# Kernel optimization log

Measured on AMD Instinct MI355X. Metric: run time of the kernel, lower is better.

The kernel has to match this reference:

```python
import jax, jax.numpy as jnp
import numpy as np
import math

# ---- static configuration (mirrors init_kwargs) ----
NQ = 8            # n_qubits (main register)
NA = 2            # n_ancilla = ceil(log2(n_select))
NSEL = 4          # n_select
DEG = 3           # degree
LAYERS = 2        # n_ansatz_layers
KLOC = 2          # k_local
LATENT = 128
B = 256
NROTS = 4 * NQ * LAYERS          # 64
GROUPS = [(s, s + 1) for s in range(NQ - KLOC + 1)]  # sliding 2-local -> 7 groups
NOBS = len(GROUPS)
KDIM = 2 ** KLOC                  # 4
C64 = jnp.complex64
TWO_PI = 2.0 * math.pi

CNOT = jnp.array([[1, 0, 0, 0], [0, 1, 0, 0], [0, 0, 0, 1], [0, 0, 1, 0]], dtype=C64)

# ---- gate matrices (theta may be traced) ----
def ry_mat(th):
    c = jnp.cos(th / 2).astype(C64); s = jnp.sin(th / 2).astype(C64)
    return jnp.stack([jnp.stack([c, -s]), jnp.stack([s, c])])

def rz_mat(th):
    return jnp.diag(jnp.stack([jnp.exp(-0.5j * th), jnp.exp(0.5j * th)])).astype(C64)

def crx_mat(th):
    c = jnp.cos(th / 2).astype(C64); isn = (-1j * jnp.sin(th / 2)).astype(C64)
    one = jnp.ones((), C64)
    m = jnp.zeros((4, 4), C64)
    m = m.at[0, 0].set(one).at[1, 1].set(one)
    m = m.at[2, 2].set(c).at[3, 3].set(c).at[2, 3].set(isn).at[3, 2].set(isn)
    return m

# ---- state-vector gate application (state: (2,)*rank, wire = axis) ----
def apply_1q(state, U, w):
    return jnp.moveaxis(jnp.tensordot(U, state, axes=((1,), (w,))), 0, w)

def apply_2q(state, U, w0, w1):
    st = jnp.tensordot(U.reshape(2, 2, 2, 2), state, axes=((2, 3), (w0, w1)))
    return jnp.moveaxis(st, (0, 1), (w0, w1))

def _sim14_ops(nq, layers):
    ops, idx = [], 0
    for _ in range(layers):
        for i in range(nq):
            ops.append(("ry", (i,), idx)); idx += 1
        for i in range(nq - 1, -1, -1):
            ops.append(("crx", (i, (i + 1) % nq), idx)); idx += 1
        for i in range(nq):
            ops.append(("ry", (i,), idx)); idx += 1
        for i in [nq - 1] + list(range(nq - 1)):
            ops.append(("crx", (i, (i - 1) % nq), idx)); idx += 1
    return ops

def apply_sim14(state, p, layers, adjoint=False):
    ops = _sim14_ops(NQ, layers)
    seq = list(reversed(ops)) if adjoint else ops
    sgn = -1.0 if adjoint else 1.0
    for kind, ws, idx in seq:
        th = sgn * p[idx]
        if kind == "ry":
            state = apply_1q(state, ry_mat(th), ws[0])
        else:
            state = apply_2q(state, crx_mat(th), ws[0], ws[1])
    return state

def pcphase(state, phi):
    # e^{+i phi} on ancilla=|0..0> subspace (first 2^NQ states in (anc, main) ordering), e^{-i phi} elsewhere
    sr = state.reshape(2 ** NQ, 2 ** NA)
    ph = jnp.where(jnp.arange(2 ** NA) == 0, jnp.exp(1j * phi), jnp.exp(-1j * phi)).astype(C64)
    return (sr * ph[None, :]).reshape(state.shape)

def prepare(state, prep_p, adjoint=False):
    if not adjoint:
        for ly in range(NA):          # n_prep_layers == n_ancilla
            for qi in range(NA):
                state = apply_1q(state, ry_mat(prep_p[ly, qi, 0]), NQ + qi)
                state = apply_1q(state, rz_mat(prep_p[ly, qi, 1]), NQ + qi)
            for i in range(NA - 1):
                state = apply_2q(state, CNOT, NQ + i, NQ + i + 1)
    else:
        for ly in reversed(range(NA)):
            for i in reversed(range(NA - 1)):
                state = apply_2q(state, CNOT, NQ + i, NQ + i + 1)
            for qi in reversed(range(NA)):
                state = apply_1q(state, rz_mat(-prep_p[ly, qi, 1]), NQ + qi)
                state = apply_1q(state, ry_mat(-prep_p[ly, qi, 0]), NQ + qi)
    return state

def select(state, ts, adjoint=False):
    # ancilla wires (NQ, NQ+1) are the trailing axes; flattened index == control value s
    sr = state.reshape((2,) * NQ + (2 ** NA,))
    for s in range(NSEL):
        sub = apply_sim14(sr[..., s], ts[s], LAYERS, adjoint=adjoint)
        sr = sr.at[..., s].set(sub)
    return sr.reshape(state.shape)

def create_hermitian(A, Bp, D, N):
    h = jnp.zeros((N, N), C64)
    count = 0
    for i in range(1, N):
        h = h.at[i - 1, i - 1].set(D[i].astype(C64))
        for j in range(i):
            h = h.at[i, j].set((A[count + j] + 1j * Bp[count + j]).astype(C64))
        count += i
    return h + h.conj().T

def simulate(ts, prep_p, sig, qff, H_all):
    # ts: (NSEL, NROTS) for one batch element
    state = jnp.zeros((2,) * (NQ + NA), C64).at[(0,) * (NQ + NA)].set(1.0)
    state = pcphase(state, sig[0])
    for k in range(DEG):
        state = prepare(state, prep_p)
        state = select(state, ts, adjoint=(k % 2 == 1))
        state = prepare(state, prep_p, adjoint=True)
        state = pcphase(state, sig[k + 1])
    state = apply_sim14(state, qff, 1)
    es = []
    for w, (a, b) in enumerate(GROUPS):
        hpsi = apply_2q(state, H_all[w], a, b)
        es.append(jnp.real(jnp.vdot(state, hpsi)))
    return jnp.stack(es).astype(jnp.float32)  # (NOBS,)

def linear(x, w, b):
    return x @ w.T + b

def sinusoidal_embedding(t, dim):
    half = dim // 2
    freqs = jnp.exp(-math.log(10000.0) * jnp.arange(half, dtype=jnp.float32) / half)
    args = t[:, None] * freqs[None]
    return jnp.concatenate([jnp.cos(args), jnp.sin(args)], axis=-1)

def _forward(z_t, t, te_w1, te_b1, te_w2, te_b2, ip_w1, ip_b1, ip_w2, ip_b2,
             prep_params, signal_angles, qff_params, A_obs, B_obs, D_obs, head_w, head_b):
    t_emb = sinusoidal_embedding(t, LATENT)
    t_emb = linear(jax.nn.silu(linear(t_emb, te_w1, te_b1)), te_w2, te_b2)
    h = jnp.concatenate([z_t, t_emb], axis=-1)
    h = linear(jax.nn.silu(linear(h, ip_w1, ip_b1)), ip_w2, ip_b2)
    ts = jax.nn.sigmoid(h).reshape(z_t.shape[0], NSEL, NROTS) * TWO_PI
    H_all = jax.vmap(lambda a, b, d: create_hermitian(a, b, d, KDIM))(A_obs, B_obs, D_obs)  # (NOBS,4,4)
    expvals = jax.vmap(simulate, in_axes=(0, None, None, None, None))(
        ts, prep_params, signal_angles, qff_params, H_all)  # (B, NOBS)
    return linear(expvals, head_w, head_b)  # (B, LATENT)

def setup_inputs() -> dict:
    key = jax.random.key(0)
    ks = jax.random.split(key, 16)
    def n(k, shape, s=0.05):
        return s * jax.random.normal(k, shape, jnp.float32)
    return {
        "z_t": jax.random.normal(ks[0], (B, LATENT), jnp.float32),
        "t": jax.random.uniform(ks[1], (B,), jnp.float32),
        "te_w1": n(ks[2], (LATENT, LATENT)), "te_b1": jnp.zeros((LATENT,), jnp.float32),
        "te_w2": n(ks[3], (LATENT, LATENT)), "te_b2": jnp.zeros((LATENT,), jnp.float32),
        "ip_w1": n(ks[4], (2 * LATENT, 2 * LATENT)), "ip_b1": jnp.zeros((2 * LATENT,), jnp.float32),
        "ip_w2": n(ks[5], (NSEL * NROTS, 2 * LATENT)), "ip_b2": jnp.zeros((NSEL * NROTS,), jnp.float32),
        "prep_params": 0.1 * jax.random.normal(ks[6], (NA, NA, 2), jnp.float32),
        "signal_angles": 0.1 * jax.random.normal(ks[7], (DEG + 1,), jnp.float32),
        "qff_params": jax.random.uniform(ks[8], (4 * NQ,), jnp.float32),
        "A_obs": 2.0 * jax.random.normal(ks[9], (NOBS, KDIM * (KDIM - 1) // 2), jnp.float32),
        "B_obs": 2.0 * jax.random.normal(ks[10], (NOBS, KDIM * (KDIM - 1) // 2), jnp.float32),
        "D_obs": 2.0 * jax.random.normal(ks[11], (NOBS, KDIM), jnp.float32),
        "head_w": n(ks[12], (LATENT, NOBS)), "head_b": jnp.zeros((LATENT,), jnp.float32),
    }

def reference(z_t, t, te_w1, te_b1, te_w2, te_b2, ip_w1, ip_b1, ip_w2, ip_b2,
              prep_params, signal_angles, qff_params, A_obs, B_obs, D_obs, head_w, head_b):
    return _forward(z_t, t, te_w1, te_b1, te_w2, te_b2, ip_w1, ip_b1, ip_w2, ip_b2,
                    prep_params, signal_angles, qff_params, A_obs, B_obs, D_obs, head_w, head_b)
```

## Files before the change

kernel.cpp:

```cpp
#include <hip/hip_runtime.h>
#include <math.h>

#define NOBS 7
#define PI_F 3.14159265358979f


template<int LM>
__device__ __forceinline__ float lane_partner(float x) {
  if constexpr (LM == 1) {
    return __int_as_float(__builtin_amdgcn_mov_dpp(__float_as_int(x), 0xB1, 0xF, 0xF, true));
  } else if constexpr (LM == 2) {
    return __int_as_float(__builtin_amdgcn_mov_dpp(__float_as_int(x), 0x4E, 0xF, 0xF, true));
  } else if constexpr (LM == 4) {
    int a = __builtin_amdgcn_mov_dpp(__float_as_int(x), 0x1B, 0xF, 0xF, true);
    return __int_as_float(__builtin_amdgcn_mov_dpp(a, 0x141, 0xF, 0xF, true));
  } else if constexpr (LM == 8) {
    int a = __builtin_amdgcn_mov_dpp(__float_as_int(x), 0x141, 0xF, 0xF, true);
    return __int_as_float(__builtin_amdgcn_mov_dpp(a, 0x140, 0xF, 0xF, true));
  } else if constexpr (LM == 16) {
#if __has_builtin(__builtin_amdgcn_permlane16_swap)
    unsigned xu = __float_as_uint(x);
    auto r = __builtin_amdgcn_permlane16_swap(xu, xu, false, false);
    return (__uint_as_float(r[0]) + __uint_as_float(r[1])) - x;
#else
    return __shfl_xor(x, 16, 64);
#endif
  } else {
#if __has_builtin(__builtin_amdgcn_permlane32_swap)
    unsigned xu = __float_as_uint(x);
    auto r = __builtin_amdgcn_permlane32_swap(xu, xu, false, false);
    return (__uint_as_float(r[0]) + __uint_as_float(r[1])) - x;
#else
    return __shfl_xor(x, 32, 64);
#endif
  }
}

template<int LM>
__device__ __forceinline__ float xor_sum(float x) {
  if constexpr (LM == 16) {
#if __has_builtin(__builtin_amdgcn_permlane16_swap)
    unsigned xu = __float_as_uint(x);
    auto r = __builtin_amdgcn_permlane16_swap(xu, xu, false, false);
    return __uint_as_float(r[0]) + __uint_as_float(r[1]);
#else
    return x + __shfl_xor(x, 16, 64);
#endif
  } else if constexpr (LM == 32) {
#if __has_builtin(__builtin_amdgcn_permlane32_swap)
    unsigned xu = __float_as_uint(x);
    auto r = __builtin_amdgcn_permlane32_swap(xu, xu, false, false);
    return __uint_as_float(r[0]) + __uint_as_float(r[1]);
#else
    return x + __shfl_xor(x, 32, 64);
#endif
  } else {
    return x + lane_partner<LM>(x);
  }
}

__device__ __forceinline__ float rdlane(float v, int idx) {
  return __int_as_float(__builtin_amdgcn_readlane(__float_as_int(v), idx));
}

__device__ __forceinline__ float2 cmul(float2 a, float2 b) {
  return make_float2(a.x*b.x - a.y*b.y, a.x*b.y + a.y*b.x);
}
__device__ __forceinline__ float2 cmulc(float2 a, float2 b) {
  return make_float2(a.x*b.x + a.y*b.y, a.y*b.x - a.x*b.y);
}
__device__ __forceinline__ float2 cadd(float2 a, float2 b) {
  return make_float2(a.x + b.x, a.y + b.y);
}

struct S4 { float r0, r1, i0, i1; };

__device__ __forceinline__ float4 wexch(int site, int wv, int lane,
                                        const float* vr, const float* vi) {
  extern __shared__ float4 dxw[];
  float4* buf = dxw + (site & 1) * 512;
  buf[wv * 64 + lane] = make_float4(vr[0], vr[1], vi[0], vi[1]);
  __syncthreads();
  return buf[(wv ^ 4) * 64 + lane];
}


template<int W>
__device__ __forceinline__ void ry_lane_g(float* vr, float* vi, int lane,
                                          float ct, float st, int idx, float sg) {
  float c = rdlane(ct, idx), s = sg * rdlane(st, idx);
  constexpr int LM = 1 << (5 - W);
  const float ls = (lane & LM) ? s : -s;
#pragma unroll
  for (int r = 0; r < 2; ++r) {
    float pr = lane_partner<LM>(vr[r]);
    float pi = lane_partner<LM>(vi[r]);
    vr[r] = c*vr[r] + ls*pr;
    vi[r] = c*vi[r] + ls*pi;
  }
}

__device__ __forceinline__ void ry_wave6_g(float* vr, float* vi, int wv, int lane, int h,
                                           float ct, float st, int idx, float sg, int site) {
  float c = rdlane(ct, idx), s = sg * rdlane(st, idx);
  float4 P = wexch(site, wv, lane, vr, vi);
  const float ls = h ? s : -s;
  vr[0] = c*vr[0] + ls*P.x;  vr[1] = c*vr[1] + ls*P.y;
  vi[0] = c*vi[0] + ls*P.z;  vi[1] = c*vi[1] + ls*P.w;
}

__device__ __forceinline__ void ry_reg7_g(float* vr, float* vi,
                                          float ct, float st, int idx, float sg) {
  float c = rdlane(ct, idx), s = sg * rdlane(st, idx);
  float a0 = vr[0], a1 = vr[1];
  vr[0] = c*a0 - s*a1;  vr[1] = s*a0 + c*a1;
  float b0 = vi[0], b1 = vi[1];
  vi[0] = c*b0 - s*b1;  vi[1] = s*b0 + c*b1;
}

template<int C, int T>
__device__ __forceinline__ void crx_ll_g(float* vr, float* vi, int lane,
                                         float ct, float st, int idx, float sg) {
  float c = rdlane(ct, idx), s = sg * rdlane(st, idx);
  constexpr int LC = 1 << (5 - C), LT = 1 << (5 - T);
  const bool act = (lane & LC) != 0;
  const float cp = act ? c : 1.f, sp = act ? s : 0.f;
#pragma unroll
  for (int r = 0; r < 2; ++r) {
    float pr = lane_partner<LT>(vr[r]);
    float pi = lane_partner<LT>(vi[r]);
    vr[r] = cp*vr[r] + sp*pi;
    vi[r] = cp*vi[r] - sp*pr;
  }
}

template<int T>
__device__ __forceinline__ void crx_7l_g(float* vr, float* vi,
                                         float ct, float st, int idx, float sg) {
  float c = rdlane(ct, idx), s = sg * rdlane(st, idx);
  constexpr int LT = 1 << (5 - T);
  float pr = lane_partner<LT>(vr[1]);
  float pi = lane_partner<LT>(vi[1]);
  vr[1] = c*vr[1] + s*pi;
  vi[1] = c*vi[1] - s*pr;
}

template<int C>
__device__ __forceinline__ void crx_l7_g(float* vr, float* vi, int lane,
                                         float ct, float st, int idx, float sg) {
  float c = rdlane(ct, idx), s = sg * rdlane(st, idx);
  constexpr int LC = 1 << (5 - C);
  const bool act = (lane & LC) != 0;
  const float cp = act ? c : 1.f, sp = act ? s : 0.f;
  float xr = vr[0], xi = vi[0], yr = vr[1], yi = vi[1];
  vr[0] = cp*xr + sp*yi;  vi[0] = cp*xi - sp*yr;
  vr[1] = cp*yr + sp*xi;  vi[1] = cp*yi - sp*xr;
}

template<int C>
__device__ __forceinline__ void crx_l6_g(float* vr, float* vi, int wv, int lane,
                                         float ct, float st, int idx, float sg, int site) {
  float c = rdlane(ct, idx), s = sg * rdlane(st, idx);
  float4 P = wexch(site, wv, lane, vr, vi);
  constexpr int LC = 1 << (5 - C);
  const bool act = (lane & LC) != 0;
  const float cp = act ? c : 1.f, sp = act ? s : 0.f;
  vr[0] = cp*vr[0] + sp*P.z;  vi[0] = cp*vi[0] - sp*P.x;
  vr[1] = cp*vr[1] + sp*P.w;  vi[1] = cp*vi[1] - sp*P.y;
}

__device__ __forceinline__ void crx_67_g(float* vr, float* vi, int h,
                                         float ct, float st, int idx, float sg) {
  if (h) {
    float c = rdlane(ct, idx), s = sg * rdlane(st, idx);
    float xr = vr[0], xi = vi[0], yr = vr[1], yi = vi[1];
    vr[0] = c*xr + s*yi;  vi[0] = c*xi - s*yr;
    vr[1] = c*yr + s*xi;  vi[1] = c*yi - s*xr;
  }
}

template<int T>
__device__ __forceinline__ void crx_6l_g(float* vr, float* vi, int h,
                                         float ct, float st, int idx, float sg) {
  if (h) {
    float c = rdlane(ct, idx), s = sg * rdlane(st, idx);
    constexpr int LT = 1 << (5 - T);
#pragma unroll
    for (int r = 0; r < 2; ++r) {
      float pr = lane_partner<LT>(vr[r]);
      float pi = lane_partner<LT>(vi[r]);
      vr[r] = c*vr[r] + s*pi;
      vi[r] = c*vi[r] - s*pr;
    }
  }
}

__device__ __forceinline__ void trio_fwd(float* vr, float* vi, int wv, int lane, int h,
                                         float ct, float st, int ia, int ib, int ic,
                                         float sg, int site) {
  float ca = rdlane(ct, ia), sa = sg * rdlane(st, ia);
  float cb = rdlane(ct, ib), sb = sg * rdlane(st, ib);
  float cc = rdlane(ct, ic), sc = sg * rdlane(st, ic);
  float4 P = wexch(site, wv, lane, vr, vi);
  const float lsa = h ? sa : -sa;
  float bor0 = ca*vr[0] + lsa*P.x, boi0 = ca*vi[0] + lsa*P.z;
  float bor1 = ca*vr[1] + lsa*P.y, boi1 = ca*vi[1] + lsa*P.w;
  float bpr0 = ca*P.x - lsa*vr[0], bpi0 = ca*P.z - lsa*vi[0];
  float bpr1 = ca*P.y - lsa*vr[1], bpi1 = ca*P.w - lsa*vi[1];
  float cor0 = cb*bor0 - sb*bor1, coi0 = cb*boi0 - sb*boi1;
  float cor1 = sb*bor0 + cb*bor1, coi1 = sb*boi0 + cb*boi1;
  float cpr1 = sb*bpr0 + cb*bpr1, cpi1 = sb*bpi0 + cb*bpi1;
  vr[0] = cor0;                 vi[0] = coi0;
  vr[1] = cc*cor1 + sc*cpi1;    vi[1] = cc*coi1 - sc*cpr1;
}

__device__ __forceinline__ void trio_adj(float* vr, float* vi, int wv, int lane, int h,
                                         float ct, float st, int ia, int ib, int ic,
                                         float sg, int site) {
  float ca = rdlane(ct, ia), sa = sg * rdlane(st, ia);
  float cb = rdlane(ct, ib), sb = sg * rdlane(st, ib);
  float cc = rdlane(ct, ic), sc = sg * rdlane(st, ic);
  float4 P = wexch(site, wv, lane, vr, vi);
  float dor1 = cc*vr[1] + sc*P.w,   doi1 = cc*vi[1] - sc*P.y;
  float dpr1 = cc*P.y + sc*vi[1],   dpi1 = cc*P.w - sc*vr[1];
  float eor0 = cb*vr[0] - sb*dor1,  eoi0 = cb*vi[0] - sb*doi1;
  float eor1 = sb*vr[0] + cb*dor1,  eoi1 = sb*vi[0] + cb*doi1;
  float epr0 = cb*P.x  - sb*dpr1,   epi0 = cb*P.z  - sb*dpi1;
  float epr1 = sb*P.x  + cb*dpr1,   epi1 = sb*P.z  + cb*dpi1;
  const float lsa = h ? sa : -sa;
  vr[0] = ca*eor0 + lsa*epr0;  vi[0] = ca*eoi0 + lsa*epi0;
  vr[1] = ca*eor1 + lsa*epr1;  vi[1] = ca*eoi1 + lsa*epi1;
}


__device__ __noinline__ S4 sim14_fwd(S4 v, float ct, float st, int off, int site0) {
  const int tid = threadIdx.x;
  const int lane = tid & 63, wv = tid >> 6, h = wv >> 2;
  float vr[2] = {v.r0, v.r1}, vi[2] = {v.i0, v.i1};
  const float sg = 1.f;
  ry_lane_g<0>(vr,vi,lane,ct,st,off+0,sg); ry_lane_g<1>(vr,vi,lane,ct,st,off+1,sg);
  ry_lane_g<2>(vr,vi,lane,ct,st,off+2,sg); ry_lane_g<3>(vr,vi,lane,ct,st,off+3,sg);
  ry_lane_g<4>(vr,vi,lane,ct,st,off+4,sg); ry_lane_g<5>(vr,vi,lane,ct,st,off+5,sg);
  ry_wave6_g(vr,vi,wv,lane,h,ct,st,off+6,sg,site0+0);
  ry_reg7_g(vr,vi,ct,st,off+7,sg);
  crx_7l_g<0>(vr,vi,ct,st,off+8,sg);
  crx_67_g(vr,vi,h,ct,st,off+9,sg);
  crx_l6_g<5>(vr,vi,wv,lane,ct,st,off+10,sg,site0+1);
  crx_ll_g<4,5>(vr,vi,lane,ct,st,off+11,sg); crx_ll_g<3,4>(vr,vi,lane,ct,st,off+12,sg);
  crx_ll_g<2,3>(vr,vi,lane,ct,st,off+13,sg); crx_ll_g<1,2>(vr,vi,lane,ct,st,off+14,sg);
  crx_ll_g<0,1>(vr,vi,lane,ct,st,off+15,sg);
  ry_lane_g<0>(vr,vi,lane,ct,st,off+16,sg); ry_lane_g<1>(vr,vi,lane,ct,st,off+17,sg);
  ry_lane_g<2>(vr,vi,lane,ct,st,off+18,sg); ry_lane_g<3>(vr,vi,lane,ct,st,off+19,sg);
  ry_lane_g<4>(vr,vi,lane,ct,st,off+20,sg); ry_lane_g<5>(vr,vi,lane,ct,st,off+21,sg);
  trio_fwd(vr,vi,wv,lane,h,ct,st,off+22,off+23,off+24,sg,site0+2);
  crx_l7_g<0>(vr,vi,lane,ct,st,off+25,sg);
  crx_ll_g<1,0>(vr,vi,lane,ct,st,off+26,sg); crx_ll_g<2,1>(vr,vi,lane,ct,st,off+27,sg);
  crx_ll_g<3,2>(vr,vi,lane,ct,st,off+28,sg); crx_ll_g<4,3>(vr,vi,lane,ct,st,off+29,sg);
  crx_ll_g<5,4>(vr,vi,lane,ct,st,off+30,sg);
  crx_6l_g<5>(vr,vi,h,ct,st,off+31,sg);
  return {vr[0], vr[1], vi[0], vi[1]};
}

__device__ __noinline__ S4 sim14_adj(S4 v, float ct, float st, int off, int site0) {
  const int tid = threadIdx.x;
  const int lane = tid & 63, wv = tid >> 6, h = wv >> 2;
  float vr[2] = {v.r0, v.r1}, vi[2] = {v.i0, v.i1};
  const float sg = -1.f;
  crx_6l_g<5>(vr,vi,h,ct,st,off+31,sg);
  crx_ll_g<5,4>(vr,vi,lane,ct,st,off+30,sg); crx_ll_g<4,3>(vr,vi,lane,ct,st,off+29,sg);
  crx_ll_g<3,2>(vr,vi,lane,ct,st,off+28,sg); crx_ll_g<2,1>(vr,vi,lane,ct,st,off+27,sg);
  crx_ll_g<1,0>(vr,vi,lane,ct,st,off+26,sg);
  crx_l7_g<0>(vr,vi,lane,ct,st,off+25,sg);
  trio_adj(vr,vi,wv,lane,h,ct,st,off+22,off+23,off+24,sg,site0+0);
  ry_lane_g<5>(vr,vi,lane,ct,st,off+21,sg); ry_lane_g<4>(vr,vi,lane,ct,st,off+20,sg);
  ry_lane_g<3>(vr,vi,lane,ct,st,off+19,sg); ry_lane_g<2>(vr,vi,lane,ct,st,off+18,sg);
  ry_lane_g<1>(vr,vi,lane,ct,st,off+17,sg); ry_lane_g<0>(vr,vi,lane,ct,st,off+16,sg);
  crx_ll_g<0,1>(vr,vi,lane,ct,st,off+15,sg); crx_ll_g<1,2>(vr,vi,lane,ct,st,off+14,sg);
  crx_ll_g<2,3>(vr,vi,lane,ct,st,off+13,sg); crx_ll_g<3,4>(vr,vi,lane,ct,st,off+12,sg);
  crx_ll_g<4,5>(vr,vi,lane,ct,st,off+11,sg);
  crx_l6_g<5>(vr,vi,wv,lane,ct,st,off+10,sg,site0+1);
  crx_67_g(vr,vi,h,ct,st,off+9,sg);
  crx_7l_g<0>(vr,vi,ct,st,off+8,sg);
  ry_reg7_g(vr,vi,ct,st,off+7,sg);
  ry_wave6_g(vr,vi,wv,lane,h,ct,st,off+6,sg,site0+2);
  ry_lane_g<5>(vr,vi,lane,ct,st,off+5,sg); ry_lane_g<4>(vr,vi,lane,ct,st,off+4,sg);
  ry_lane_g<3>(vr,vi,lane,ct,st,off+3,sg); ry_lane_g<2>(vr,vi,lane,ct,st,off+2,sg);
  ry_lane_g<1>(vr,vi,lane,ct,st,off+1,sg); ry_lane_g<0>(vr,vi,lane,ct,st,off+0,sg);
  return {vr[0], vr[1], vi[0], vi[1]};
}


template<int IN, int NP, int MODE>
__device__ __forceinline__ void mlp_layer(const float* __restrict__ W,
    const float* __restrict__ bias, const float* xl, float* yl,
    int rbase, int lane)
{
  const int sub = lane & 7;
  const int g   = lane >> 3;
#pragma unroll
  for (int p = 0; p < NP; ++p) {
    const int row = rbase + p * 8 + g;
    const float4* w4 = (const float4*)(W + row * IN) + sub;
    const float4* x4 = (const float4*)xl + sub;
    float acc = 0.f;
#pragma unroll
    for (int it = 0; it < IN / 32; ++it) {
      float4 w = w4[it * 8], e = x4[it * 8];
      acc += w.x*e.x + w.y*e.y + w.z*e.z + w.w*e.w;
    }
    acc = xor_sum<1>(acc);
    acc = xor_sum<2>(acc);
    acc = xor_sum<4>(acc);
    if (sub == 0) {
      float a = acc + bias[row];
      if constexpr (MODE == 0) {
        yl[row] = a / (1.f + __expf(-a));
      } else if constexpr (MODE == 1) {
        yl[row] = a;
      } else {
        float th = PI_F / (1.f + __expf(-a));
        float sn, cn;
        __sincosf(th, &sn, &cn);
        ((float2*)yl)[row] = make_float2(cn, sn);
      }
    }
  }
}


__global__ __launch_bounds__(512) void qsvt_kernel(
    const float* __restrict__ z_t, const float* __restrict__ t,
    const float* __restrict__ te_w1, const float* __restrict__ te_b1,
    const float* __restrict__ te_w2, const float* __restrict__ te_b2,
    const float* __restrict__ ip_w1, const float* __restrict__ ip_b1,
    const float* __restrict__ ip_w2, const float* __restrict__ ip_b2,
    const float* __restrict__ prep_p, const float* __restrict__ sig,
    const float* __restrict__ qff,
    const float* __restrict__ A_obs, const float* __restrict__ B_obs,
    const float* __restrict__ D_obs,
    const float* __restrict__ head_w, const float* __restrict__ head_b,
    float* __restrict__ out)
{
  __shared__ __align__(16) float emb[128];
  __shared__ __align__(16) float y1[128];
  __shared__ __align__(16) float hbuf[256];
  __shared__ __align__(16) float h1[256];
  __shared__ __align__(16) float2 seltab[256];
  __shared__ __align__(16) float2 qtab2[32];
  __shared__ __align__(16) float2 sX1[16], sX2[16], sF[16], sa0[4];
  __shared__ __align__(16) float dumpR[4][256];
  __shared__ __align__(16) float dumpI[4][256];
  __shared__ float redbuf[NOBS][4];
  __shared__ float hdc[NOBS][3], hxc[NOBS][6], hyc[NOBS][6];
  __shared__ __align__(16) float shw[128 * NOBS];
  __shared__ __align__(16) float shb[128];
  extern __shared__ float4 dxw[];

  const int tid  = threadIdx.x;
  const int lane = tid & 63;
  const int wv   = tid >> 6;
  const int s    = wv & 3;
  const int h    = wv >> 2;
  const int b    = blockIdx.x;

  if (tid < 32) {
    float sn, cn;
    __sincosf(0.5f * qff[tid], &sn, &cn);
    qtab2[tid] = make_float2(cn, sn);
  }
  if (wv == 0) {
    float2 Ga[2][2][2], Gb[2][2][2];
    for (int ly = 0; ly < 2; ++ly)
      for (int qi = 0; qi < 2; ++qi) {
        float y = prep_p[ly*4 + qi*2 + 0], z = prep_p[ly*4 + qi*2 + 1];
        float cy, sy, cz, sz;
        __sincosf(0.5f*y, &sy, &cy);
        __sincosf(0.5f*z, &sz, &cz);
        float2 g00 = make_float2( cy*cz, -cy*sz);
        float2 g01 = make_float2(-sy*cz,  sy*sz);
        float2 g10 = make_float2( sy*cz,  sy*sz);
        float2 g11 = make_float2( cy*cz,  cy*sz);
        if (qi == 0) { Ga[ly][0][0]=g00; Ga[ly][0][1]=g01; Ga[ly][1][0]=g10; Ga[ly][1][1]=g11; }
        else         { Gb[ly][0][0]=g00; Gb[ly][0][1]=g01; Gb[ly][1][0]=g10; Gb[ly][1][1]=g11; }
      }
    float2 M[2][4][4];
    for (int ly = 0; ly < 2; ++ly) {
      float2 T[4][4];
      for (int i = 0; i < 4; ++i)
        for (int j = 0; j < 4; ++j)
          T[i][j] = cmul(Ga[ly][i>>1][j>>1], Gb[ly][i&1][j&1]);
      for (int j = 0; j < 4; ++j) {
        M[ly][0][j] = T[0][j]; M[ly][1][j] = T[1][j];
        M[ly][2][j] = T[3][j]; M[ly][3][j] = T[2][j];
      }
    }
    float2 U[4][4];
    for (int i = 0; i < 4; ++i)
      for (int j = 0; j < 4; ++j) {
        float2 acc = make_float2(0.f, 0.f);
        for (int kk = 0; kk < 4; ++kk) acc = cadd(acc, cmul(M[1][i][kk], M[0][kk][j]));
        U[i][j] = acc;
      }
    float c0n, s0n, c1, s1v, c2, s2v, c3, s3v;
    __sincosf(sig[0], &s0n, &c0n);
    __sincosf(sig[1], &s1v, &c1);
    __sincosf(sig[2], &s2v, &c2);
    __sincosf(sig[3], &s3v, &c3);
    if (lane < 16) {
      int i = lane >> 2, j = lane & 3;
      float2 a1 = make_float2(0.f, 0.f), a2 = make_float2(0.f, 0.f);
      for (int k = 0; k < 4; ++k) {
        float2 tt = cmulc(U[i][k], U[j][k]);
        float sk = (k == 0) ? 1.f : -1.f;
        a1 = cadd(a1, cmul(tt, make_float2(c1, sk*s1v)));
        a2 = cadd(a2, cmul(tt, make_float2(c2, sk*s2v)));
      }
      sX1[lane] = a1;
      sX2[lane] = a2;
      float2 d3 = make_float2(c3, (i == 0) ? s3v : -s3v);
      sF[lane] = cmul(d3, make_float2(U[j][i].x, -U[j][i].y));
    }
    if (lane < 4) sa0[lane] = cmul(U[lane][0], make_float2(c0n, s0n));
  }

  if (tid < 128) {
    float fr = __expf(-9.210340371976184f * (float)(tid & 63) / 64.f);
    float arg = t[b] * fr;
    float sn, cn;
    __sincosf(arg, &sn, &cn);
    emb[tid] = (tid < 64) ? cn : sn;
  }
  __syncthreads();

  mlp_layer<128, 2, 0>(te_w1, te_b1, emb, y1, wv * 16, lane);
  if (tid < 128) hbuf[tid] = z_t[b * 128 + tid];
  __syncthreads();

  mlp_layer<128, 2, 1>(te_w2, te_b2, y1, hbuf + 128, wv * 16, lane);
  __syncthreads();

  mlp_layer<256, 4, 0>(ip_w1, ip_b1, hbuf, h1, wv * 32, lane);
  __syncthreads();

  mlp_layer<256, 4, 2>(ip_w2, ip_b2, h1, (float*)seltab, wv * 32, lane);

  if (tid < NOBS * 6)      { hxc[tid/6][tid%6] = A_obs[tid]; hyc[tid/6][tid%6] = B_obs[tid]; }
  else if (tid >= 64 && tid < 64 + NOBS*3) { int q = tid - 64; hdc[q/3][q%3] = 2.f * D_obs[(q/3)*4 + (q%3) + 1]; }
#pragma unroll
  for (int i = tid; i < 128*NOBS; i += 512) shw[i] = head_w[i];
  if (tid < 128) shb[tid] = head_b[tid];
  __syncthreads();

  float2 mycs = seltab[(s << 6) | lane];
  float selc = mycs.x, sels = mycs.y;
  float2 myq = qtab2[lane & 31];
  float qc = myq.x, qs = myq.y;

  S4 v;
  v.r0 = 0.f; v.r1 = 0.f; v.i0 = 0.f; v.i1 = 0.f;
  if (lane == 0 && h == 0) {
    float2 a0 = sa0[s];
    v.r0 = a0.x; v.i0 = a0.y;
  }

  auto ancmix = [&](const float2* R, int site) {
    float4* buf = dxw + (site & 1) * 512;
    buf[wv * 64 + lane] = make_float4(v.r0, v.r1, v.i0, v.i1);
    __syncthreads();
    float2 o0 = make_float2(0.f, 0.f), o1 = make_float2(0.f, 0.f);
#pragma unroll
    for (int sp = 0; sp < 4; ++sp) {
      float4 P = buf[(h * 4 + sp) * 64 + lane];
      float2 Rr = R[sp];
      o0 = cadd(o0, cmul(Rr, make_float2(P.x, P.z)));
      o1 = cadd(o1, cmul(Rr, make_float2(P.y, P.w)));
    }
    v.r0 = o0.x; v.i0 = o0.y; v.r1 = o1.x; v.i1 = o1.y;
  };

  v = sim14_fwd(v, selc, sels, 0, 0);
  v = sim14_fwd(v, selc, sels, 32, 3);
  ancmix(&sX1[s << 2], 6);
  v = sim14_adj(v, selc, sels, 32, 7);
  v = sim14_adj(v, selc, sels, 0, 10);
  ancmix(&sX2[s << 2], 13);
  v = sim14_fwd(v, selc, sels, 0, 14);
  v = sim14_fwd(v, selc, sels, 32, 17);
  ancmix(&sF[s << 2], 20);
  v = sim14_fwd(v, qc, qs, 0, 21);

  *(float2*)&dumpR[s][(lane << 2) | (h << 1)] = make_float2(v.r0, v.r1);
  *(float2*)&dumpI[s][(lane << 2) | (h << 1)] = make_float2(v.i0, v.i1);
  __syncthreads();

  const int w0 = h ? 4 : 0, w1 = h ? NOBS : 4;
  for (int w = w0; w < w1; ++w) {
    const int pb = 6 - w;
    int g = lane;
    int ib = ((g >> pb) << (pb + 2)) | (g & ((1 << pb) - 1));
    float xr[4], xi[4];
#pragma unroll
    for (int i = 0; i < 4; ++i) { xr[i] = dumpR[s][ib + (i << pb)]; xi[i] = dumpI[s][ib + (i << pb)]; }
    float a = hdc[w][0] * (xr[0]*xr[0] + xi[0]*xi[0])
            + hdc[w][1] * (xr[1]*xr[1] + xi[1]*xi[1])
            + hdc[w][2] * (xr[2]*xr[2] + xi[2]*xi[2]);
    const int oi[6] = {1, 2, 2, 3, 3, 3};
    const int oj[6] = {0, 0, 1, 0, 1, 2};
#pragma unroll
    for (int k2 = 0; k2 < 6; ++k2) {
      int i = oi[k2], j = oj[k2];
      float rr = xr[i]*xr[j] + xi[i]*xi[j];
      float ii = xr[i]*xi[j] - xi[i]*xr[j];
      a += 2.f * (hxc[w][k2]*rr - hyc[w][k2]*ii);
    }
    a = xor_sum<32>(a);
    a = xor_sum<16>(a);
    a = xor_sum<8>(a);
    a = xor_sum<4>(a);
    a = xor_sum<2>(a);
    a = xor_sum<1>(a);
    if (lane == 0) redbuf[w][s] = a;
  }
  __syncthreads();

  if (tid < 128) {
    float acc = shb[tid];
#pragma unroll
    for (int w = 0; w < NOBS; ++w) {
      float ev = redbuf[w][0] + redbuf[w][1] + redbuf[w][2] + redbuf[w][3];
      acc += ev * shw[tid*NOBS + w];
    }
    out[b * 128 + tid] = acc;
  }
}

extern "C" void kernel_launch(void* const* d_in, const int* in_sizes, int n_in,
                              void* d_out, int out_size, void* d_ws, size_t ws_size,
                              hipStream_t stream) {
  (void)n_in; (void)out_size; (void)d_ws; (void)ws_size;
  const float* z_t    = (const float*)d_in[0];
  const float* t      = (const float*)d_in[1];
  const float* te_w1  = (const float*)d_in[2];
  const float* te_b1  = (const float*)d_in[3];
  const float* te_w2  = (const float*)d_in[4];
  const float* te_b2  = (const float*)d_in[5];
  const float* ip_w1  = (const float*)d_in[6];
  const float* ip_b1  = (const float*)d_in[7];
  const float* ip_w2  = (const float*)d_in[8];
  const float* ip_b2  = (const float*)d_in[9];
  const float* prep_p = (const float*)d_in[10];
  const float* sig    = (const float*)d_in[11];
  const float* qff    = (const float*)d_in[12];
  const float* A_obs  = (const float*)d_in[13];
  const float* B_obs  = (const float*)d_in[14];
  const float* D_obs  = (const float*)d_in[15];
  const float* head_w = (const float*)d_in[16];
  const float* head_b = (const float*)d_in[17];
  float* out = (float*)d_out;

  int B = in_sizes[1];
  size_t dyn = 2 * 512 * sizeof(float4);
  qsvt_kernel<<<B, 512, dyn, stream>>>(
      z_t, t, te_w1, te_b1, te_w2, te_b2, ip_w1, ip_b1, ip_w2, ip_b2,
      prep_p, sig, qff, A_obs, B_obs, D_obs, head_w, head_b, out);
}
```

Baseline: 125.2 us.

## Map each select branch to a single wave with four amplitudes per lane

Switches from 8 waves (two per select branch) to 4 waves per block. Each lane now holds four amplitudes, so qubits 6 and 7 live in registers. The LDS exchanges and block-wide barriers needed for gates on qubit 6 are gone, along with the barrier before the observable stage. MLP layers now give each wave twice as many rows, which trades thread-level parallelism and raises register pressure in the serial MLP phase.

After: 126.5 us. Within noise of the previous version (+1.0%).

```diff
diff --git a/kernel.cpp b/kernel.cpp
--- a/kernel.cpp
+++ b/kernel.cpp
@@ -73,26 +73,17 @@
   return make_float2(a.x + b.x, a.y + b.y);
 }
 
-struct S4 { float r0, r1, i0, i1; };
-
-__device__ __forceinline__ float4 wexch(int site, int wv, int lane,
-                                        const float* vr, const float* vi) {
-  extern __shared__ float4 dxw[];
-  float4* buf = dxw + (site & 1) * 512;
-  buf[wv * 64 + lane] = make_float4(vr[0], vr[1], vi[0], vi[1]);
-  __syncthreads();
-  return buf[(wv ^ 4) * 64 + lane];
-}
+struct S8 { float r[4]; float i[4]; };
 
 
 template<int W>
-__device__ __forceinline__ void ry_lane_g(float* vr, float* vi, int lane,
-                                          float ct, float st, int idx, float sg) {
+__device__ __forceinline__ void ry_lane4(float* vr, float* vi, int lane,
+                                         float ct, float st, int idx, float sg) {
   float c = rdlane(ct, idx), s = sg * rdlane(st, idx);
   constexpr int LM = 1 << (5 - W);
   const float ls = (lane & LM) ? s : -s;
 #pragma unroll
-  for (int r = 0; r < 2; ++r) {
+  for (int r = 0; r < 4; ++r) {
     float pr = lane_partner<LM>(vr[r]);
     float pi = lane_partner<LM>(vi[r]);
     vr[r] = c*vr[r] + ls*pr;
@@ -100,33 +91,39 @@
   }
 }
 
-__device__ __forceinline__ void ry_wave6_g(float* vr, float* vi, int wv, int lane, int h,
-                                           float ct, float st, int idx, float sg, int site) {
-  float c = rdlane(ct, idx), s = sg * rdlane(st, idx);
-  float4 P = wexch(site, wv, lane, vr, vi);
-  const float ls = h ? s : -s;
-  vr[0] = c*vr[0] + ls*P.x;  vr[1] = c*vr[1] + ls*P.y;
-  vi[0] = c*vi[0] + ls*P.z;  vi[1] = c*vi[1] + ls*P.w;
-}
-
-__device__ __forceinline__ void ry_reg7_g(float* vr, float* vi,
-                                          float ct, float st, int idx, float sg) {
-  float c = rdlane(ct, idx), s = sg * rdlane(st, idx);
-  float a0 = vr[0], a1 = vr[1];
-  vr[0] = c*a0 - s*a1;  vr[1] = s*a0 + c*a1;
-  float b0 = vi[0], b1 = vi[1];
-  vi[0] = c*b0 - s*b1;  vi[1] = s*b0 + c*b1;
+__device__ __forceinline__ void ry_reg6(float* vr, float* vi,
+                                        float ct, float st, int idx, float sg) {
+  float c = rdlane(ct, idx), s = sg * rdlane(st, idx);
+#pragma unroll
+  for (int k = 0; k < 2; ++k) {
+    float a0 = vr[k], a1 = vr[k + 2];
+    vr[k] = c*a0 - s*a1;  vr[k + 2] = s*a0 + c*a1;
+    float b0 = vi[k], b1 = vi[k + 2];
+    vi[k] = c*b0 - s*b1;  vi[k + 2] = s*b0 + c*b1;
+  }
+}
+
+__device__ __forceinline__ void ry_reg7(float* vr, float* vi,
+                                        float ct, float st, int idx, float sg) {
+  float c = rdlane(ct, idx), s = sg * rdlane(st, idx);
+#pragma unroll
+  for (int k = 0; k < 4; k += 2) {
+    float a0 = vr[k], a1 = vr[k + 1];
+    vr[k] = c*a0 - s*a1;  vr[k + 1] = s*a0 + c*a1;
+    float b0 = vi[k], b1 = vi[k + 1];
+    vi[k] = c*b0 - s*b1;  vi[k + 1] = s*b0 + c*b1;
+  }
 }
 
 template<int C, int T>
-__device__ __forceinline__ void crx_ll_g(float* vr, float* vi, int lane,
-                                         float ct, float st, int idx, float sg) {
+__device__ __forceinline__ void crx_ll4(float* vr, float* vi, int lane,
+                                        float ct, float st, int idx, float sg) {
   float c = rdlane(ct, idx), s = sg * rdlane(st, idx);
   constexpr int LC = 1 << (5 - C), LT = 1 << (5 - T);
   const bool act = (lane & LC) != 0;
   const float cp = act ? c : 1.f, sp = act ? s : 0.f;
 #pragma unroll
-  for (int r = 0; r < 2; ++r) {
+  for (int r = 0; r < 4; ++r) {
     float pr = lane_partner<LT>(vr[r]);
     float pi = lane_partner<LT>(vi[r]);
     vr[r] = cp*vr[r] + sp*pi;
@@ -134,59 +131,14 @@
   }
 }
 
-template<int T>
-__device__ __forceinline__ void crx_7l_g(float* vr, float* vi,
-                                         float ct, float st, int idx, float sg) {
+template<int RB, int T>
+__device__ __forceinline__ void crx_rc_lane(float* vr, float* vi,
+                                            float ct, float st, int idx, float sg) {
   float c = rdlane(ct, idx), s = sg * rdlane(st, idx);
   constexpr int LT = 1 << (5 - T);
-  float pr = lane_partner<LT>(vr[1]);
-  float pi = lane_partner<LT>(vi[1]);
-  vr[1] = c*vr[1] + s*pi;
-  vi[1] = c*vi[1] - s*pr;
-}
-
-template<int C>
-__device__ __forceinline__ void crx_l7_g(float* vr, float* vi, int lane,
-                                         float ct, float st, int idx, float sg) {
-  float c = rdlane(ct, idx), s = sg * rdlane(st, idx);
-  constexpr int LC = 1 << (5 - C);
-  const bool act = (lane & LC) != 0;
-  const float cp = act ? c : 1.f, sp = act ? s : 0.f;
-  float xr = vr[0], xi = vi[0], yr = vr[1], yi = vi[1];
-  vr[0] = cp*xr + sp*yi;  vi[0] = cp*xi - sp*yr;
-  vr[1] = cp*yr + sp*xi;  vi[1] = cp*yi - sp*xr;
-}
-
-template<int C>
-__device__ __forceinline__ void crx_l6_g(float* vr, float* vi, int wv, int lane,
-                                         float ct, float st, int idx, float sg, int site) {
-  float c = rdlane(ct, idx), s = sg * rdlane(st, idx);
-  float4 P = wexch(site, wv, lane, vr, vi);
-  constexpr int LC = 1 << (5 - C);
-  const bool act = (lane & LC) != 0;
-  const float cp = act ? c : 1.f, sp = act ? s : 0.f;
-  vr[0] = cp*vr[0] + sp*P.z;  vi[0] = cp*vi[0] - sp*P.x;
-  vr[1] = cp*vr[1] + sp*P.w;  vi[1] = cp*vi[1] - sp*P.y;
-}
-
-__device__ __forceinline__ void crx_67_g(float* vr, float* vi, int h,
-                                         float ct, float st, int idx, float sg) {
-  if (h) {
-    float c = rdlane(ct, idx), s = sg * rdlane(st, idx);
-    float xr = vr[0], xi = vi[0], yr = vr[1], yi = vi[1];
-    vr[0] = c*xr + s*yi;  vi[0] = c*xi - s*yr;
-    vr[1] = c*yr + s*xi;  vi[1] = c*yi - s*xr;
-  }
-}
-
-template<int T>
-__device__ __forceinline__ void crx_6l_g(float* vr, float* vi, int h,
-                                         float ct, float st, int idx, float sg) {
-  if (h) {
-    float c = rdlane(ct, idx), s = sg * rdlane(st, idx);
-    constexpr int LT = 1 << (5 - T);
-#pragma unroll
-    for (int r = 0; r < 2; ++r) {
+#pragma unroll
+  for (int r = 0; r < 4; ++r) {
+    if (r & RB) {
       float pr = lane_partner<LT>(vr[r]);
       float pi = lane_partner<LT>(vi[r]);
       vr[r] = c*vr[r] + s*pi;
@@ -195,98 +147,99 @@
   }
 }
 
-__device__ __forceinline__ void trio_fwd(float* vr, float* vi, int wv, int lane, int h,
-                                         float ct, float st, int ia, int ib, int ic,
-                                         float sg, int site) {
-  float ca = rdlane(ct, ia), sa = sg * rdlane(st, ia);
-  float cb = rdlane(ct, ib), sb = sg * rdlane(st, ib);
-  float cc = rdlane(ct, ic), sc = sg * rdlane(st, ic);
-  float4 P = wexch(site, wv, lane, vr, vi);
-  const float lsa = h ? sa : -sa;
-  float bor0 = ca*vr[0] + lsa*P.x, boi0 = ca*vi[0] + lsa*P.z;
-  float bor1 = ca*vr[1] + lsa*P.y, boi1 = ca*vi[1] + lsa*P.w;
-  float bpr0 = ca*P.x - lsa*vr[0], bpi0 = ca*P.z - lsa*vi[0];
-  float bpr1 = ca*P.y - lsa*vr[1], bpi1 = ca*P.w - lsa*vi[1];
-  float cor0 = cb*bor0 - sb*bor1, coi0 = cb*boi0 - sb*boi1;
-  float cor1 = sb*bor0 + cb*bor1, coi1 = sb*boi0 + cb*boi1;
-  float cpr1 = sb*bpr0 + cb*bpr1, cpi1 = sb*bpi0 + cb*bpi1;
-  vr[0] = cor0;                 vi[0] = coi0;
-  vr[1] = cc*cor1 + sc*cpi1;    vi[1] = cc*coi1 - sc*cpr1;
-}
-
-__device__ __forceinline__ void trio_adj(float* vr, float* vi, int wv, int lane, int h,
-                                         float ct, float st, int ia, int ib, int ic,
-                                         float sg, int site) {
-  float ca = rdlane(ct, ia), sa = sg * rdlane(st, ia);
-  float cb = rdlane(ct, ib), sb = sg * rdlane(st, ib);
-  float cc = rdlane(ct, ic), sc = sg * rdlane(st, ic);
-  float4 P = wexch(site, wv, lane, vr, vi);
-  float dor1 = cc*vr[1] + sc*P.w,   doi1 = cc*vi[1] - sc*P.y;
-  float dpr1 = cc*P.y + sc*vi[1],   dpi1 = cc*P.w - sc*vr[1];
-  float eor0 = cb*vr[0] - sb*dor1,  eoi0 = cb*vi[0] - sb*doi1;
-  float eor1 = sb*vr[0] + cb*dor1,  eoi1 = sb*vi[0] + cb*doi1;
-  float epr0 = cb*P.x  - sb*dpr1,   epi0 = cb*P.z  - sb*dpi1;
-  float epr1 = sb*P.x  + cb*dpr1,   epi1 = sb*P.z  + cb*dpi1;
-  const float lsa = h ? sa : -sa;
-  vr[0] = ca*eor0 + lsa*epr0;  vi[0] = ca*eoi0 + lsa*epi0;
-  vr[1] = ca*eor1 + lsa*epr1;  vi[1] = ca*eoi1 + lsa*epi1;
-}
-
-
-__device__ __noinline__ S4 sim14_fwd(S4 v, float ct, float st, int off, int site0) {
-  const int tid = threadIdx.x;
-  const int lane = tid & 63, wv = tid >> 6, h = wv >> 2;
-  float vr[2] = {v.r0, v.r1}, vi[2] = {v.i0, v.i1};
+template<int C, int TB>
+__device__ __forceinline__ void crx_lc_reg(float* vr, float* vi, int lane,
+                                           float ct, float st, int idx, float sg) {
+  float c = rdlane(ct, idx), s = sg * rdlane(st, idx);
+  constexpr int LC = 1 << (5 - C);
+  const bool act = (lane & LC) != 0;
+  const float cp = act ? c : 1.f, sp = act ? s : 0.f;
+#pragma unroll
+  for (int x = 0; x < 4; ++x) {
+    if (!(x & TB)) {
+      const int y = x | TB;
+      float xr = vr[x], xi = vi[x], yr = vr[y], yi = vi[y];
+      vr[x] = cp*xr + sp*yi;  vi[x] = cp*xi - sp*yr;
+      vr[y] = cp*yr + sp*xi;  vi[y] = cp*yi - sp*xr;
+    }
+  }
+}
+
+template<int CB, int TB>
+__device__ __forceinline__ void crx_rr(float* vr, float* vi,
+                                       float ct, float st, int idx, float sg) {
+  float c = rdlane(ct, idx), s = sg * rdlane(st, idx);
+  constexpr int x = CB, y = CB | TB;
+  float xr = vr[x], xi = vi[x], yr = vr[y], yi = vi[y];
+  vr[x] = c*xr + s*yi;  vi[x] = c*xi - s*yr;
+  vr[y] = c*yr + s*xi;  vi[y] = c*yi - s*xr;
+}
+
+
+__device__ __noinline__ S8 sim14_fwd(S8 v, float ct, float st, int off) {
+  const int lane = threadIdx.x & 63;
+  float vr[4] = {v.r[0], v.r[1], v.r[2], v.r[3]};
+  float vi[4] = {v.i[0], v.i[1], v.i[2], v.i[3]};
   const float sg = 1.f;
-  ry_lane_g<0>(vr,vi,lane,ct,st,off+0,sg); ry_lane_g<1>(vr,vi,lane,ct,st,off+1,sg);
-  ry_lane_g<2>(vr,vi,lane,ct,st,off+2,sg); ry_lane_g<3>(vr,vi,lane,ct,st,off+3,sg);
-  ry_lane_g<4>(vr,vi,lane,ct,st,off+4,sg); ry_lane_g<5>(vr,vi,lane,ct,st,off+5,sg);
-  ry_wave6_g(vr,vi,wv,lane,h,ct,st,off+6,sg,site0+0);
-  ry_reg7_g(vr,vi,ct,st,off+7,sg);
-  crx_7l_g<0>(vr,vi,ct,st,off+8,sg);
-  crx_67_g(vr,vi,h,ct,st,off+9,sg);
-  crx_l6_g<5>(vr,vi,wv,lane,ct,st,off+10,sg,site0+1);
-  crx_ll_g<4,5>(vr,vi,lane,ct,st,off+11,sg); crx_ll_g<3,4>(vr,vi,lane,ct,st,off+12,sg);
-  crx_ll_g<2,3>(vr,vi,lane,ct,st,off+13,sg); crx_ll_g<1,2>(vr,vi,lane,ct,st,off+14,sg);
-  crx_ll_g<0,1>(vr,vi,lane,ct,st,off+15,sg);
-  ry_lane_g<0>(vr,vi,lane,ct,st,off+16,sg); ry_lane_g<1>(vr,vi,lane,ct,st,off+17,sg);
-  ry_lane_g<2>(vr,vi,lane,ct,st,off+18,sg); ry_lane_g<3>(vr,vi,lane,ct,st,off+19,sg);
-  ry_lane_g<4>(vr,vi,lane,ct,st,off+20,sg); ry_lane_g<5>(vr,vi,lane,ct,st,off+21,sg);
-  trio_fwd(vr,vi,wv,lane,h,ct,st,off+22,off+23,off+24,sg,site0+2);
-  crx_l7_g<0>(vr,vi,lane,ct,st,off+25,sg);
-  crx_ll_g<1,0>(vr,vi,lane,ct,st,off+26,sg); crx_ll_g<2,1>(vr,vi,lane,ct,st,off+27,sg);
-  crx_ll_g<3,2>(vr,vi,lane,ct,st,off+28,sg); crx_ll_g<4,3>(vr,vi,lane,ct,st,off+29,sg);
-  crx_ll_g<5,4>(vr,vi,lane,ct,st,off+30,sg);
-  crx_6l_g<5>(vr,vi,h,ct,st,off+31,sg);
-  return {vr[0], vr[1], vi[0], vi[1]};
-}
-
-__device__ __noinline__ S4 sim14_adj(S4 v, float ct, float st, int off, int site0) {
-  const int tid = threadIdx.x;
-  const int lane = tid & 63, wv = tid >> 6, h = wv >> 2;
-  float vr[2] = {v.r0, v.r1}, vi[2] = {v.i0, v.i1};
+  ry_lane4<0>(vr,vi,lane,ct,st,off+0,sg); ry_lane4<1>(vr,vi,lane,ct,st,off+1,sg);
+  ry_lane4<2>(vr,vi,lane,ct,st,off+2,sg); ry_lane4<3>(vr,vi,lane,ct,st,off+3,sg);
+  ry_lane4<4>(vr,vi,lane,ct,st,off+4,sg); ry_lane4<5>(vr,vi,lane,ct,st,off+5,sg);
+  ry_reg6(vr,vi,ct,st,off+6,sg);
+  ry_reg7(vr,vi,ct,st,off+7,sg);
+  crx_rc_lane<1,0>(vr,vi,ct,st,off+8,sg);
+  crx_rr<2,1>(vr,vi,ct,st,off+9,sg);
+  crx_lc_reg<5,2>(vr,vi,lane,ct,st,off+10,sg);
+  crx_ll4<4,5>(vr,vi,lane,ct,st,off+11,sg); crx_ll4<3,4>(vr,vi,lane,ct,st,off+12,sg);
+  crx_ll4<2,3>(vr,vi,lane,ct,st,off+13,sg); crx_ll4<1,2>(vr,vi,lane,ct,st,off+14,sg);
+  crx_ll4<0,1>(vr,vi,lane,ct,st,off+15,sg);
+  ry_lane4<0>(vr,vi,lane,ct,st,off+16,sg); ry_lane4<1>(vr,vi,lane,ct,st,off+17,sg);
+  ry_lane4<2>(vr,vi,lane,ct,st,off+18,sg); ry_lane4<3>(vr,vi,lane,ct,st,off+19,sg);
+  ry_lane4<4>(vr,vi,lane,ct,st,off+20,sg); ry_lane4<5>(vr,vi,lane,ct,st,off+21,sg);
+  ry_reg6(vr,vi,ct,st,off+22,sg);
+  ry_reg7(vr,vi,ct,st,off+23,sg);
+  crx_rr<1,2>(vr,vi,ct,st,off+24,sg);
+  crx_lc_reg<0,1>(vr,vi,lane,ct,st,off+25,sg);
+  crx_ll4<1,0>(vr,vi,lane,ct,st,off+26,sg); crx_ll4<2,1>(vr,vi,lane,ct,st,off+27,sg);
+  crx_ll4<3,2>(vr,vi,lane,ct,st,off+28,sg); crx_ll4<4,3>(vr,vi,lane,ct,st,off+29,sg);
+  crx_ll4<5,4>(vr,vi,lane,ct,st,off+30,sg);
+  crx_rc_lane<2,5>(vr,vi,ct,st,off+31,sg);
+  S8 o;
+#pragma unroll
+  for (int r = 0; r < 4; ++r) { o.r[r] = vr[r]; o.i[r] = vi[r]; }
+  return o;
+}
+
+__device__ __noinline__ S8 sim14_adj(S8 v, float ct, float st, int off) {
+  const int lane = threadIdx.x & 63;
+  float vr[4] = {v.r[0], v.r[1], v.r[2], v.r[3]};
+  float vi[4] = {v.i[0], v.i[1], v.i[2], v.i[3]};
   const float sg = -1.f;
-  crx_6l_g<5>(vr,vi,h,ct,st,off+31,sg);
-  crx_ll_g<5,4>(vr,vi,lane,ct,st,off+30,sg); crx_ll_g<4,3>(vr,vi,lane,ct,st,off+29,sg);
-  crx_ll_g<3,2>(vr,vi,lane,ct,st,off+28,sg); crx_ll_g<2,1>(vr,vi,lane,ct,st,off+27,sg);
-  crx_ll_g<1,0>(vr,vi,lane,ct,st,off+26,sg);
-  crx_l7_g<0>(vr,vi,lane,ct,st,off+25,sg);
-  trio_adj(vr,vi,wv,lane,h,ct,st,off+22,off+23,off+24,sg,site0+0);
-  ry_lane_g<5>(vr,vi,lane,ct,st,off+21,sg); ry_lane_g<4>(vr,vi,lane,ct,st,off+20,sg);
-  ry_lane_g<3>(vr,vi,lane,ct,st,off+19,sg); ry_lane_g<2>(vr,vi,lane,ct,st,off+18,sg);
-  ry_lane_g<1>(vr,vi,lane,ct,st,off+17,sg); ry_lane_g<0>(vr,vi,lane,ct,st,off+16,sg);
-  crx_ll_g<0,1>(vr,vi,lane,ct,st,off+15,sg); crx_ll_g<1,2>(vr,vi,lane,ct,st,off+14,sg);
-  crx_ll_g<2,3>(vr,vi,lane,ct,st,off+13,sg); crx_ll_g<3,4>(vr,vi,lane,ct,st,off+12,sg);
-  crx_ll_g<4,5>(vr,vi,lane,ct,st,off+11,sg);
-  crx_l6_g<5>(vr,vi,wv,lane,ct,st,off+10,sg,site0+1);
-  crx_67_g(vr,vi,h,ct,st,off+9,sg);
-  crx_7l_g<0>(vr,vi,ct,st,off+8,sg);
-  ry_reg7_g(vr,vi,ct,st,off+7,sg);
-  ry_wave6_g(vr,vi,wv,lane,h,ct,st,off+6,sg,site0+2);
-  ry_lane_g<5>(vr,vi,lane,ct,st,off+5,sg); ry_lane_g<4>(vr,vi,lane,ct,st,off+4,sg);
-  ry_lane_g<3>(vr,vi,lane,ct,st,off+3,sg); ry_lane_g<2>(vr,vi,lane,ct,st,off+2,sg);
-  ry_lane_g<1>(vr,vi,lane,ct,st,off+1,sg); ry_lane_g<0>(vr,vi,lane,ct,st,off+0,sg);
-  return {vr[0], vr[1], vi[0], vi[1]};
+  crx_rc_lane<2,5>(vr,vi,ct,st,off+31,sg);
+  crx_ll4<5,4>(vr,vi,lane,ct,st,off+30,sg); crx_ll4<4,3>(vr,vi,lane,ct,st,off+29,sg);
+  crx_ll4<3,2>(vr,vi,lane,ct,st,off+28,sg); crx_ll4<2,1>(vr,vi,lane,ct,st,off+27,sg);
+  crx_ll4<1,0>(vr,vi,lane,ct,st,off+26,sg);
+  crx_lc_reg<0,1>(vr,vi,lane,ct,st,off+25,sg);
+  crx_rr<1,2>(vr,vi,ct,st,off+24,sg);
+  ry_reg7(vr,vi,ct,st,off+23,sg);
+  ry_reg6(vr,vi,ct,st,off+22,sg);
+  ry_lane4<5>(vr,vi,lane,ct,st,off+21,sg); ry_lane4<4>(vr,vi,lane,ct,st,off+20,sg);
+  ry_lane4<3>(vr,vi,lane,ct,st,off+19,sg); ry_lane4<2>(vr,vi,lane,ct,st,off+18,sg);
+  ry_lane4<1>(vr,vi,lane,ct,st,off+17,sg); ry_lane4<0>(vr,vi,lane,ct,st,off+16,sg);
+  crx_ll4<0,1>(vr,vi,lane,ct,st,off+15,sg); crx_ll4<1,2>(vr,vi,lane,ct,st,off+14,sg);
+  crx_ll4<2,3>(vr,vi,lane,ct,st,off+13,sg); crx_ll4<3,4>(vr,vi,lane,ct,st,off+12,sg);
+  crx_ll4<4,5>(vr,vi,lane,ct,st,off+11,sg);
+  crx_lc_reg<5,2>(vr,vi,lane,ct,st,off+10,sg);
+  crx_rr<2,1>(vr,vi,ct,st,off+9,sg);
+  crx_rc_lane<1,0>(vr,vi,ct,st,off+8,sg);
+  ry_reg7(vr,vi,ct,st,off+7,sg);
+  ry_reg6(vr,vi,ct,st,off+6,sg);
+  ry_lane4<5>(vr,vi,lane,ct,st,off+5,sg); ry_lane4<4>(vr,vi,lane,ct,st,off+4,sg);
+  ry_lane4<3>(vr,vi,lane,ct,st,off+3,sg); ry_lane4<2>(vr,vi,lane,ct,st,off+2,sg);
+  ry_lane4<1>(vr,vi,lane,ct,st,off+1,sg); ry_lane4<0>(vr,vi,lane,ct,st,off+0,sg);
+  S8 o;
+#pragma unroll
+  for (int r = 0; r < 4; ++r) { o.r[r] = vr[r]; o.i[r] = vi[r]; }
+  return o;
 }
 
 
@@ -328,7 +281,7 @@
 }
 
 
-__global__ __launch_bounds__(512) void qsvt_kernel(
+__global__ __launch_bounds__(256) void qsvt_kernel(
     const float* __restrict__ z_t, const float* __restrict__ t,
     const float* __restrict__ te_w1, const float* __restrict__ te_b1,
     const float* __restrict__ te_w2, const float* __restrict__ te_b2,
@@ -359,8 +312,7 @@
   const int tid  = threadIdx.x;
   const int lane = tid & 63;
   const int wv   = tid >> 6;
-  const int s    = wv & 3;
-  const int h    = wv >> 2;
+  const int s    = wv;
   const int b    = blockIdx.x;
 
   if (tid < 32) {
@@ -432,22 +384,22 @@
   }
   __syncthreads();
 
-  mlp_layer<128, 2, 0>(te_w1, te_b1, emb, y1, wv * 16, lane);
+  mlp_layer<128, 4, 0>(te_w1, te_b1, emb, y1, wv * 32, lane);
   if (tid < 128) hbuf[tid] = z_t[b * 128 + tid];
   __syncthreads();
 
-  mlp_layer<128, 2, 1>(te_w2, te_b2, y1, hbuf + 128, wv * 16, lane);
+  mlp_layer<128, 4, 1>(te_w2, te_b2, y1, hbuf + 128, wv * 32, lane);
   __syncthreads();
 
-  mlp_layer<256, 4, 0>(ip_w1, ip_b1, hbuf, h1, wv * 32, lane);
+  mlp_layer<256, 8, 0>(ip_w1, ip_b1, hbuf, h1, wv * 64, lane);
   __syncthreads();
 
-  mlp_layer<256, 4, 2>(ip_w2, ip_b2, h1, (float*)seltab, wv * 32, lane);
+  mlp_layer<256, 8, 2>(ip_w2, ip_b2, h1, (float*)seltab, wv * 64, lane);
 
   if (tid < NOBS * 6)      { hxc[tid/6][tid%6] = A_obs[tid]; hyc[tid/6][tid%6] = B_obs[tid]; }
   else if (tid >= 64 && tid < 64 + NOBS*3) { int q = tid - 64; hdc[q/3][q%3] = 2.f * D_obs[(q/3)*4 + (q%3) + 1]; }
 #pragma unroll
-  for (int i = tid; i < 128*NOBS; i += 512) shw[i] = head_w[i];
+  for (int i = tid; i < 128*NOBS; i += 256) shw[i] = head_w[i];
   if (tid < 128) shb[tid] = head_b[tid];
   __syncthreads();
 
@@ -456,45 +408,51 @@
   float2 myq = qtab2[lane & 31];
   float qc = myq.x, qs = myq.y;
 
-  S4 v;
-  v.r0 = 0.f; v.r1 = 0.f; v.i0 = 0.f; v.i1 = 0.f;
-  if (lane == 0 && h == 0) {
+  S8 v;
+#pragma unroll
+  for (int r = 0; r < 4; ++r) { v.r[r] = 0.f; v.i[r] = 0.f; }
+  if (lane == 0) {
     float2 a0 = sa0[s];
-    v.r0 = a0.x; v.i0 = a0.y;
+    v.r[0] = a0.x; v.i[0] = a0.y;
   }
 
   auto ancmix = [&](const float2* R, int site) {
-    float4* buf = dxw + (site & 1) * 512;
-    buf[wv * 64 + lane] = make_float4(v.r0, v.r1, v.i0, v.i1);
+    float4* bufR = dxw + (site & 1) * 512;
+    float4* bufI = bufR + 256;
+    bufR[wv * 64 + lane] = make_float4(v.r[0], v.r[1], v.r[2], v.r[3]);
+    bufI[wv * 64 + lane] = make_float4(v.i[0], v.i[1], v.i[2], v.i[3]);
     __syncthreads();
-    float2 o0 = make_float2(0.f, 0.f), o1 = make_float2(0.f, 0.f);
+    float outr[4] = {0.f, 0.f, 0.f, 0.f}, outi[4] = {0.f, 0.f, 0.f, 0.f};
 #pragma unroll
     for (int sp = 0; sp < 4; ++sp) {
-      float4 P = buf[(h * 4 + sp) * 64 + lane];
+      float4 Pr = bufR[sp * 64 + lane];
+      float4 Pi = bufI[sp * 64 + lane];
       float2 Rr = R[sp];
-      o0 = cadd(o0, cmul(Rr, make_float2(P.x, P.z)));
-      o1 = cadd(o1, cmul(Rr, make_float2(P.y, P.w)));
-    }
-    v.r0 = o0.x; v.i0 = o0.y; v.r1 = o1.x; v.i1 = o1.y;
+      outr[0] += Rr.x*Pr.x - Rr.y*Pi.x;  outi[0] += Rr.x*Pi.x + Rr.y*Pr.x;
+      outr[1] += Rr.x*Pr.y - Rr.y*Pi.y;  outi[1] += Rr.x*Pi.y + Rr.y*Pr.y;
+      outr[2] += Rr.x*Pr.z - Rr.y*Pi.z;  outi[2] += Rr.x*Pi.z + Rr.y*Pr.z;
+      outr[3] += Rr.x*Pr.w - Rr.y*Pi.w;  outi[3] += Rr.x*Pi.w + Rr.y*Pr.w;
+    }
+#pragma unroll
+    for (int r = 0; r < 4; ++r) { v.r[r] = outr[r]; v.i[r] = outi[r]; }
   };
 
-  v = sim14_fwd(v, selc, sels, 0, 0);
-  v = sim14_fwd(v, selc, sels, 32, 3);
-  ancmix(&sX1[s << 2], 6);
-  v = sim14_adj(v, selc, sels, 32, 7);
-  v = sim14_adj(v, selc, sels, 0, 10);
-  ancmix(&sX2[s << 2], 13);
-  v = sim14_fwd(v, selc, sels, 0, 14);
-  v = sim14_fwd(v, selc, sels, 32, 17);
-  ancmix(&sF[s << 2], 20);
-  v = sim14_fwd(v, qc, qs, 0, 21);
-
-  *(float2*)&dumpR[s][(lane << 2) | (h << 1)] = make_float2(v.r0, v.r1);
-  *(float2*)&dumpI[s][(lane << 2) | (h << 1)] = make_float2(v.i0, v.i1);
-  __syncthreads();
-
-  const int w0 = h ? 4 : 0, w1 = h ? NOBS : 4;
-  for (int w = w0; w < w1; ++w) {
+  v = sim14_fwd(v, selc, sels, 0);
+  v = sim14_fwd(v, selc, sels, 32);
+  ancmix(&sX1[s << 2], 0);
+  v = sim14_adj(v, selc, sels, 32);
+  v = sim14_adj(v, selc, sels, 0);
+  ancmix(&sX2[s << 2], 1);
+  v = sim14_fwd(v, selc, sels, 0);
+  v = sim14_fwd(v, selc, sels, 32);
+  ancmix(&sF[s << 2], 2);
+  v = sim14_fwd(v, qc, qs, 0);
+
+  *(float4*)&dumpR[s][lane << 2] = make_float4(v.r[0], v.r[1], v.r[2], v.r[3]);
+  *(float4*)&dumpI[s][lane << 2] = make_float4(v.i[0], v.i[1], v.i[2], v.i[3]);
+
+#pragma unroll
+  for (int w = 0; w < NOBS; ++w) {
     const int pb = 6 - w;
     int g = lane;
     int ib = ((g >> pb) << (pb + 2)) | (g & ((1 << pb) - 1));
@@ -560,7 +518,7 @@
 
   int B = in_sizes[1];
   size_t dyn = 2 * 512 * sizeof(float4);
-  qsvt_kernel<<<B, 512, dyn, stream>>>(
+  qsvt_kernel<<<B, 256, dyn, stream>>>(
       z_t, t, te_w1, te_b1, te_w2, te_b2, ip_w1, ip_b1, ip_w2, ip_b2,
       prep_p, sig, qff, A_obs, B_obs, D_obs, head_w, head_b, out);
 }
```
